# Kernel optimization log

Hardware: AMD Instinct MI355X
Metric: run time of the kernel (lower is better)

The kernel has to match this reference:

```python
import jax, jax.numpy as jnp
import numpy as np

N_NODES = 100000
N_RELS = 237
N_EDGES = 500000
D_IN = 128
D_HID = 128
D_OUT = 128


def setup_inputs() -> dict:
    key = jax.random.key(0)
    ks = jax.random.split(key, 13)
    src = jax.random.randint(ks[0], (N_EDGES,), 0, N_NODES, dtype=jnp.int32)
    dst = jax.random.randint(ks[1], (N_EDGES,), 0, N_NODES, dtype=jnp.int32)
    rel = jax.random.randint(ks[2], (N_EDGES,), 0, N_RELS, dtype=jnp.int32)
    triplets = jnp.stack([src, dst, rel], axis=1)  # [E, 3]
    s = 0.05
    return {
        "triplets": triplets,
        "ent_embed": jax.random.normal(ks[3], (N_NODES, D_IN), jnp.float32) * s,
        "rel_embed": jax.random.normal(ks[4], (N_RELS, D_IN), jnp.float32) * s,
        "W_ent": jax.random.normal(ks[5], (D_IN, D_HID), jnp.float32) * s,
        "b_ent": jnp.zeros((D_HID,), jnp.float32),
        "W_rel": jax.random.normal(ks[6], (D_IN, D_HID), jnp.float32) * s,
        "b_rel": jnp.zeros((D_HID,), jnp.float32),
        "W_ent2": jax.random.normal(ks[7], (3 * D_HID, D_OUT), jnp.float32) * s,
        "b_ent2": jnp.zeros((D_OUT,), jnp.float32),
        "a_w": jax.random.normal(ks[8], (D_OUT, 1), jnp.float32) * s,
        "a_b": jnp.zeros((1,), jnp.float32),
    }


def reference(triplets, ent_embed, rel_embed, W_ent, b_ent, W_rel, b_rel,
              W_ent2, b_ent2, a_w, a_b):
    src_i, dst_i, rel_i = triplets[:, 0], triplets[:, 1], triplets[:, 2]
    # embedding gathers
    src = ent_embed[src_i]          # [E, D_IN]
    dst = ent_embed[dst_i]          # [E, D_IN]
    rel = rel_embed[rel_i]          # [E, D_IN]
    # shared fc_ent projection on src and dst, fc_rel on rel
    src = src @ W_ent + b_ent       # [E, D_HID]
    dst = dst @ W_ent + b_ent
    rel = rel @ W_rel + b_rel
    # per-edge feature c = fc_ent2(cat([src, dst, rel]))
    c = jnp.concatenate([src, dst, rel], axis=1) @ W_ent2 + b_ent2  # [E, D_OUT]
    # unnormalized exp attention score (leaky_relu slope 0.01, torch default)
    b = jnp.exp(jax.nn.leaky_relu((c @ a_w + a_b)[:, 0], negative_slope=0.01))  # [E]
    # segment softmax over edges sharing a source node
    b_sum = jax.ops.segment_sum(b, src_i, num_segments=N_NODES)  # [N]
    alpha = b / b_sum[src_i]                                     # [E]
    # weighted neighbor aggregation per source node
    h = jax.ops.segment_sum(alpha[:, None] * c, src_i, num_segments=N_NODES)  # [N, D_OUT]
    return h
```

## Files before the change

### kernel.cpp

```cpp
#include <hip/hip_runtime.h>
#include <hip/hip_bf16.h>

#define N_NODES_C 100000
#define N_PAD_C   100096
#define N_RELS_C  237
#define N_EDGES_C 500000
#define D 128

typedef __attribute__((ext_vector_type(8))) short short8;
typedef __attribute__((ext_vector_type(4))) float f32x4;

__device__ __forceinline__ ushort f2bf(float x) {
    union { float f; uint u; } v; v.f = x;
    uint r = v.u + 0x7FFFu + ((v.u >> 16) & 1u);
    return (ushort)(r >> 16);
}
__device__ __forceinline__ float bf2f_hi(uint u) {
    union { uint u; float f; } v; v.u = u; return v.f;
}

__global__ void k_fuse_w(const float* __restrict__ W_ent, const float* __restrict__ W_rel,
                         const float* __restrict__ W_ent2,
                         const float* __restrict__ b_ent, const float* __restrict__ b_rel,
                         const float* __restrict__ b_ent2,
                         float* __restrict__ WR, ushort* __restrict__ WfTb,
                         float* __restrict__ biasC) {
    int j = threadIdx.x;
    int k = blockIdx.x;
    int which = blockIdx.y;
    if (which == 0) {
        float acc = 0.f;
        for (int i = 0; i < D; ++i) acc += W_ent[k*D+i] * W_ent2[i*D+j];
        WfTb[j*D + k] = f2bf(acc);
    } else if (which == 1) {
        float acc = 0.f;
        for (int i = 0; i < D; ++i) acc += W_ent[k*D+i] * W_ent2[(D+i)*D+j];
        WfTb[(D+j)*D + k] = f2bf(acc);
    } else if (which == 2) {
        float acc = 0.f;
        for (int i = 0; i < D; ++i) acc += W_rel[k*D+i] * W_ent2[(2*D+i)*D+j];
        WR[k*D + j] = acc;
    } else if (k == 0) {
        float acc = b_ent2[j];
        for (int i = 0; i < D; ++i) {
            acc += b_ent[i] * (W_ent2[i*D+j] + W_ent2[(D+i)*D+j]);
            acc += b_rel[i] * W_ent2[(2*D+i)*D+j];
        }
        biasC[j] = acc;
    }
}

__global__ void k_rel_scalars(const float* __restrict__ rel_embed,
                              const float* __restrict__ a_w, const float* __restrict__ a_b,
                              const float* __restrict__ WR, const float* __restrict__ biasC,
                              float* __restrict__ Rm, float* __restrict__ sR,
                              float* __restrict__ sConst) {
    int j = threadIdx.x;
    int b = blockIdx.x;
    __shared__ float red[128];
    if (b < N_RELS_C) {
        float acc = 0.f;
        for (int k = 0; k < D; ++k) acc += rel_embed[b*D+k] * WR[k*D+j];
        Rm[b*D+j] = acc;
        red[j] = acc * a_w[j];
        __syncthreads();
        for (int s = 64; s > 0; s >>= 1) { if (j < s) red[j] += red[j+s]; __syncthreads(); }
        if (j == 0) sR[b] = red[0];
    } else {
        red[j] = biasC[j] * a_w[j];
        __syncthreads();
        for (int s = 64; s > 0; s >>= 1) { if (j < s) red[j] += red[j+s]; __syncthreads(); }
        if (j == 0) sConst[0] = red[0] + a_b[0];
    }
}

__global__ __launch_bounds__(512, 4) void k1_mfma(const float* __restrict__ ent,
                                                  const ushort* __restrict__ WfTb,
                                                  const float* __restrict__ a_w,
                                                  ushort* __restrict__ AnB,
                                                  ushort* __restrict__ BnB,
                                                  float* __restrict__ sA,
                                                  float* __restrict__ sB,
                                                  int n_nodes) {
    __shared__ __align__(16) ushort wL[256*128];
    int tid = threadIdx.x;
    int m0 = blockIdx.x * 128;

#pragma unroll
    for (int u = 0; u < 8; ++u) {
        int f = u*512 + tid;
        int r = f >> 4, k16 = f & 15;
        *(uint4*)&wL[r*128 + ((k16 ^ (r & 15)) << 3)] =
            *(const uint4*)&WfTb[r*128 + (k16 << 3)];
    }
    __syncthreads();

    int wave = tid >> 6, lane = tid & 63;
    int ny = wave >> 2;
    int q = lane >> 4, c = lane & 15;
    int wm = (wave & 3) * 32;

    f32x4 acc[2][8];
#pragma unroll
    for (int mt = 0; mt < 2; ++mt)
#pragma unroll
        for (int nt = 0; nt < 8; ++nt) { f32x4 z = {0.f,0.f,0.f,0.f}; acc[mt][nt] = z; }

#pragma unroll
    for (int chunk = 0; chunk < 4; ++chunk) {
        int k16 = chunk*4 + q;
        short8 a[2];
#pragma unroll
        for (int mt = 0; mt < 2; ++mt) {
            int row = m0 + wm + mt*16 + c;
            float4 e0 = make_float4(0.f,0.f,0.f,0.f), e1 = e0;
            if (row < n_nodes) {
                const float* ep = &ent[(size_t)row*D + (k16 << 3)];
                e0 = *(const float4*)ep;
                e1 = *(const float4*)(ep + 4);
            }
            short8 pk;
            pk[0]=(short)f2bf(e0.x); pk[1]=(short)f2bf(e0.y); pk[2]=(short)f2bf(e0.z); pk[3]=(short)f2bf(e0.w);
            pk[4]=(short)f2bf(e1.x); pk[5]=(short)f2bf(e1.y); pk[6]=(short)f2bf(e1.z); pk[7]=(short)f2bf(e1.w);
            a[mt] = pk;
        }
#pragma unroll
        for (int nt = 0; nt < 8; ++nt) {
            int wrow = ny*128 + nt*16 + c;
            short8 b = *(const short8*)&wL[wrow*128 + ((k16 ^ c) << 3)];
            acc[0][nt] = __builtin_amdgcn_mfma_f32_16x16x32_bf16(a[0], b, acc[0][nt], 0, 0, 0);
            acc[1][nt] = __builtin_amdgcn_mfma_f32_16x16x32_bf16(a[1], b, acc[1][nt], 0, 0, 0);
        }
    }

    float aw[8];
#pragma unroll
    for (int nt = 0; nt < 8; ++nt) aw[nt] = a_w[nt*16 + c];

    ushort* out  = ny ? BnB : AnB;
    float*  sOut = ny ? sB  : sA;

#pragma unroll
    for (int mt = 0; mt < 2; ++mt) {
#pragma unroll
        for (int reg = 0; reg < 4; ++reg) {
            int m = m0 + wm + mt*16 + q*4 + reg;
            float pa = 0.f;
#pragma unroll
            for (int nt = 0; nt < 8; ++nt) pa += acc[mt][nt][reg] * aw[nt];
#pragma unroll
            for (int msk = 1; msk < 16; msk <<= 1) pa += __shfl_xor(pa, msk);
            if (m < n_nodes) {
                if (c == 0) sOut[m] = pa;
#pragma unroll
                for (int nt = 0; nt < 8; ++nt)
                    out[(size_t)m*D + nt*16 + c] = f2bf(acc[mt][nt][reg]);
            }
        }
    }
}

__global__ void k_hist(const int* __restrict__ trip, int* __restrict__ deg, int n_edges) {
    int e = blockIdx.x*256 + threadIdx.x;
    if (e >= n_edges) return;
    int s = trip[3*e];
    if ((unsigned)s >= (unsigned)N_NODES_C) return;
    atomicAdd(&deg[s], 1);
}

__global__ void k_scan1(const int* __restrict__ deg, int* __restrict__ off,
                        int* __restrict__ bsum, int n) {
    __shared__ int s[1024];
    int i = blockIdx.x*1024 + threadIdx.x;
    int v = (i < n) ? deg[i] : 0;
    s[threadIdx.x] = v; __syncthreads();
    for (int d = 1; d < 1024; d <<= 1) {
        int t = (threadIdx.x >= d) ? s[threadIdx.x - d] : 0;
        __syncthreads();
        s[threadIdx.x] += t;
        __syncthreads();
    }
    if (i < n) off[i] = s[threadIdx.x] - v;
    if (threadIdx.x == 1023) bsum[blockIdx.x] = s[1023];
}

__global__ void k_scan2(int* __restrict__ bsum, int nb) {
    __shared__ int s[128];
    int v = (threadIdx.x < nb) ? bsum[threadIdx.x] : 0;
    s[threadIdx.x] = v; __syncthreads();
    for (int d = 1; d < 128; d <<= 1) {
        int t = (threadIdx.x >= d) ? s[threadIdx.x - d] : 0;
        __syncthreads();
        s[threadIdx.x] += t;
        __syncthreads();
    }
    if (threadIdx.x < nb) bsum[threadIdx.x] = s[threadIdx.x] - v;
}

__global__ void k_scan3(int* __restrict__ off, int* __restrict__ cursor,
                        const int* __restrict__ bsum, int n, int total_edges) {
    int i = blockIdx.x*1024 + threadIdx.x;
    if (i < n) {
        int o = off[i] + bsum[blockIdx.x];
        off[i] = o;
        cursor[i] = o;
    }
    if (i == 0) off[n] = total_edges;
}

__global__ void k_edge_b(const int* __restrict__ trip, const float* __restrict__ sA,
                         const float* __restrict__ sB, const float* __restrict__ sR,
                         const float* __restrict__ sConst, int* __restrict__ cursor,
                         uint2* __restrict__ kb, int n_edges) {
    int e = blockIdx.x*256 + threadIdx.x;
    if (e >= n_edges) return;
    int s = trip[3*e], d = trip[3*e+1], r = trip[3*e+2];
    if ((unsigned)s >= (unsigned)N_NODES_C || (unsigned)d >= (unsigned)N_NODES_C ||
        (unsigned)r >= (unsigned)N_RELS_C) return;
    float logit = sA[s] + sB[d] + sR[r] + sConst[0];
    float l = logit > 0.f ? logit : 0.01f*logit;
    float b = expf(l);
    int p = atomicAdd(&cursor[s], 1);
    kb[p] = make_uint2((uint)(d | (r << 20)), __float_as_uint(b));
}

__global__ void k_aggregate(const int* __restrict__ off, const uint2* __restrict__ kb,
                            const ushort* __restrict__ AnB, const ushort* __restrict__ BnB,
                            const float* __restrict__ Rm, const float* __restrict__ biasC,
                            float* __restrict__ h, int n_nodes) {
    int g = threadIdx.x >> 5, lane = threadIdx.x & 31;
    int n = blockIdx.x*8 + g;
    if (n >= n_nodes) return;
    int o0 = off[n], o1 = off[n+1];
    int c = lane*4;
    if (o0 == o1) {
        *(float4*)&h[(size_t)n*D + c] = make_float4(0.f,0.f,0.f,0.f);
        return;
    }
    float s = 0.f;
    for (int p = o0 + lane; p < o1; p += 32) s += __uint_as_float(kb[p].y);
    for (int m = 16; m > 0; m >>= 1) s += __shfl_xor(s, m, 32);
    float inv = 1.f / s;
    uint2 araw = *(const uint2*)&AnB[(size_t)n*D + c];
    float4 bc  = *(const float4*)&biasC[c];
    float4 acc;
    acc.x = bf2f_hi(araw.x << 16)         + bc.x;
    acc.y = bf2f_hi(araw.x & 0xFFFF0000u) + bc.y;
    acc.z = bf2f_hi(araw.y << 16)         + bc.z;
    acc.w = bf2f_hi(araw.y & 0xFFFF0000u) + bc.w;

    int p = o0;
    for (; p + 4 <= o1; p += 4) {
        uint2 kv0 = kb[p+0], kv1 = kb[p+1], kv2 = kb[p+2], kv3 = kb[p+3];
        uint2 g0 = *(const uint2*)&BnB[(size_t)(kv0.x & 0xFFFFF)*D + c];
        uint2 g1 = *(const uint2*)&BnB[(size_t)(kv1.x & 0xFFFFF)*D + c];
        uint2 g2 = *(const uint2*)&BnB[(size_t)(kv2.x & 0xFFFFF)*D + c];
        uint2 g3 = *(const uint2*)&BnB[(size_t)(kv3.x & 0xFFFFF)*D + c];
        float4 r0 = *(const float4*)&Rm[(kv0.x >> 20)*D + c];
        float4 r1 = *(const float4*)&Rm[(kv1.x >> 20)*D + c];
        float4 r2 = *(const float4*)&Rm[(kv2.x >> 20)*D + c];
        float4 r3 = *(const float4*)&Rm[(kv3.x >> 20)*D + c];
        float a0 = __uint_as_float(kv0.y) * inv;
        float a1 = __uint_as_float(kv1.y) * inv;
        float a2 = __uint_as_float(kv2.y) * inv;
        float a3 = __uint_as_float(kv3.y) * inv;
        acc.x += a0*(bf2f_hi(g0.x << 16)         + r0.x)
               + a1*(bf2f_hi(g1.x << 16)         + r1.x)
               + a2*(bf2f_hi(g2.x << 16)         + r2.x)
               + a3*(bf2f_hi(g3.x << 16)         + r3.x);
        acc.y += a0*(bf2f_hi(g0.x & 0xFFFF0000u) + r0.y)
               + a1*(bf2f_hi(g1.x & 0xFFFF0000u) + r1.y)
               + a2*(bf2f_hi(g2.x & 0xFFFF0000u) + r2.y)
               + a3*(bf2f_hi(g3.x & 0xFFFF0000u) + r3.y);
        acc.z += a0*(bf2f_hi(g0.y << 16)         + r0.z)
               + a1*(bf2f_hi(g1.y << 16)         + r1.z)
               + a2*(bf2f_hi(g2.y << 16)         + r2.z)
               + a3*(bf2f_hi(g3.y << 16)         + r3.z);
        acc.w += a0*(bf2f_hi(g0.y & 0xFFFF0000u) + r0.w)
               + a1*(bf2f_hi(g1.y & 0xFFFF0000u) + r1.w)
               + a2*(bf2f_hi(g2.y & 0xFFFF0000u) + r2.w)
               + a3*(bf2f_hi(g3.y & 0xFFFF0000u) + r3.w);
    }
    for (; p < o1; ++p) {
        uint2 kv = kb[p];
        float al = __uint_as_float(kv.y) * inv;
        uint2 braw = *(const uint2*)&BnB[(size_t)(kv.x & 0xFFFFF)*D + c];
        float4 rv  = *(const float4*)&Rm[(kv.x >> 20)*D + c];
        acc.x += al*(bf2f_hi(braw.x << 16)         + rv.x);
        acc.y += al*(bf2f_hi(braw.x & 0xFFFF0000u) + rv.y);
        acc.z += al*(bf2f_hi(braw.y << 16)         + rv.z);
        acc.w += al*(bf2f_hi(braw.y & 0xFFFF0000u) + rv.w);
    }
    *(float4*)&h[(size_t)n*D + c] = acc;
}

extern "C" void kernel_launch(void* const* d_in, const int* in_sizes, int n_in,
                              void* d_out, int out_size, void* d_ws, size_t ws_size,
                              hipStream_t stream) {
    const int*   trip   = (const int*)  d_in[0];
    const float* ent    = (const float*)d_in[1];
    const float* relE   = (const float*)d_in[2];
    const float* W_ent  = (const float*)d_in[3];
    const float* b_ent  = (const float*)d_in[4];
    const float* W_rel  = (const float*)d_in[5];
    const float* b_rel  = (const float*)d_in[6];
    const float* W_ent2 = (const float*)d_in[7];
    const float* b_ent2 = (const float*)d_in[8];
    const float* a_w    = (const float*)d_in[9];
    const float* a_b    = (const float*)d_in[10];
    float* h = (float*)d_out;

    char* ws = (char*)d_ws;
    size_t o = 0;
    auto alloc = [&](size_t bytes) { size_t p = o; o += (bytes + 255) & ~(size_t)255; return p; };
    float*  WR     = (float*) (ws + alloc(128*128*4));
    ushort* WfTb   = (ushort*)(ws + alloc(256*128*2));
    float*  biasC  = (float*) (ws + alloc(128*4));
    float*  Rm     = (float*) (ws + alloc((size_t)N_RELS_C*128*4));
    float*  sR     = (float*) (ws + alloc(N_RELS_C*4));
    float*  sConst = (float*) (ws + alloc(4));
    float*  sA     = (float*) (ws + alloc((size_t)N_NODES_C*4));
    float*  sB     = (float*) (ws + alloc((size_t)N_NODES_C*4));
    int*    deg    = (int*)   (ws + alloc((size_t)N_NODES_C*4));
    int*    off    = (int*)   (ws + alloc(((size_t)N_NODES_C+1)*4));
    int*    cursor = (int*)   (ws + alloc((size_t)N_NODES_C*4));
    int*    bsum   = (int*)   (ws + alloc(128*4));
    uint2*  kb     = (uint2*) (ws + alloc((size_t)N_EDGES_C*8));
    ushort* BnB    = (ushort*)(ws + alloc((size_t)N_PAD_C*128*2));
    ushort* AnB    = (ushort*)(ws + alloc((size_t)N_PAD_C*128*2));

    hipMemsetAsync(deg, 0, (size_t)N_NODES_C*4, stream);

    k_fuse_w<<<dim3(128,4), 128, 0, stream>>>(W_ent, W_rel, W_ent2, b_ent, b_rel, b_ent2,
                                              WR, WfTb, biasC);
    k_rel_scalars<<<N_RELS_C+1, 128, 0, stream>>>(relE, a_w, a_b, WR, biasC,
                                                  Rm, sR, sConst);
    k1_mfma<<<N_PAD_C/128, 512, 0, stream>>>(ent, WfTb, a_w, AnB, BnB, sA, sB, N_NODES_C);
    k_hist<<<(N_EDGES_C+255)/256, 256, 0, stream>>>(trip, deg, N_EDGES_C);
    int nb = (N_NODES_C + 1023)/1024;
    k_scan1<<<nb, 1024, 0, stream>>>(deg, off, bsum, N_NODES_C);
    k_scan2<<<1, 128, 0, stream>>>(bsum, nb);
    k_scan3<<<nb, 1024, 0, stream>>>(off, cursor, bsum, N_NODES_C, N_EDGES_C);
    k_edge_b<<<(N_EDGES_C+255)/256, 256, 0, stream>>>(trip, sA, sB, sR, sConst,
                                                      cursor, kb, N_EDGES_C);
    k_aggregate<<<(N_NODES_C+7)/8, 256, 0, stream>>>(off, kb, AnB, BnB, Rm, biasC,
                                                     h, N_NODES_C);
}
```

Before: 248.2 us.

## Fuse softmax exp into aggregation, bf16 relation table, 16 lanes per node

The edge kernel now stores only the partial logit sB[d]+sR[r]. The aggregation kernel adds the per-node term, applies leaky-relu and exp, and accumulates numerator and denominator in a single pass, so the separate sum pass over kb is gone. The relation matrix is stored as bf16 to halve gather bytes. Each node now uses 16 lanes with 8 columns apiece and 128-bit loads. The cost is exp computed redundantly by every lane and slightly lower precision in the relation term.

```diff
diff --git a/kernel.cpp b/kernel.cpp
--- a/kernel.cpp
+++ b/kernel.cpp
@@ -53,7 +53,7 @@
 __global__ void k_rel_scalars(const float* __restrict__ rel_embed,
                               const float* __restrict__ a_w, const float* __restrict__ a_b,
                               const float* __restrict__ WR, const float* __restrict__ biasC,
-                              float* __restrict__ Rm, float* __restrict__ sR,
+                              ushort* __restrict__ RmB, float* __restrict__ sR,
                               float* __restrict__ sConst) {
     int j = threadIdx.x;
     int b = blockIdx.x;
@@ -61,7 +61,7 @@
     if (b < N_RELS_C) {
         float acc = 0.f;
         for (int k = 0; k < D; ++k) acc += rel_embed[b*D+k] * WR[k*D+j];
-        Rm[b*D+j] = acc;
+        RmB[b*D+j] = f2bf(acc);
         red[j] = acc * a_w[j];
         __syncthreads();
         for (int s = 64; s > 0; s >>= 1) { if (j < s) red[j] += red[j+s]; __syncthreads(); }
@@ -208,90 +208,99 @@
     if (i == 0) off[n] = total_edges;
 }
 
-__global__ void k_edge_b(const int* __restrict__ trip, const float* __restrict__ sA,
-                         const float* __restrict__ sB, const float* __restrict__ sR,
-                         const float* __restrict__ sConst, int* __restrict__ cursor,
+__global__ void k_edge_b(const int* __restrict__ trip, const float* __restrict__ sB,
+                         const float* __restrict__ sR, int* __restrict__ cursor,
                          uint2* __restrict__ kb, int n_edges) {
     int e = blockIdx.x*256 + threadIdx.x;
     if (e >= n_edges) return;
     int s = trip[3*e], d = trip[3*e+1], r = trip[3*e+2];
     if ((unsigned)s >= (unsigned)N_NODES_C || (unsigned)d >= (unsigned)N_NODES_C ||
         (unsigned)r >= (unsigned)N_RELS_C) return;
-    float logit = sA[s] + sB[d] + sR[r] + sConst[0];
-    float l = logit > 0.f ? logit : 0.01f*logit;
-    float b = expf(l);
+    float v = sB[d] + sR[r];
     int p = atomicAdd(&cursor[s], 1);
-    kb[p] = make_uint2((uint)(d | (r << 20)), __float_as_uint(b));
+    kb[p] = make_uint2((uint)(d | (r << 20)), __float_as_uint(v));
 }
 
 __global__ void k_aggregate(const int* __restrict__ off, const uint2* __restrict__ kb,
                             const ushort* __restrict__ AnB, const ushort* __restrict__ BnB,
-                            const float* __restrict__ Rm, const float* __restrict__ biasC,
+                            const ushort* __restrict__ RmB, const float* __restrict__ biasC,
+                            const float* __restrict__ sA, const float* __restrict__ sConst,
                             float* __restrict__ h, int n_nodes) {
-    int g = threadIdx.x >> 5, lane = threadIdx.x & 31;
-    int n = blockIdx.x*8 + g;
+    int g = threadIdx.x >> 4, lane = threadIdx.x & 15;
+    int n = blockIdx.x*16 + g;
     if (n >= n_nodes) return;
     int o0 = off[n], o1 = off[n+1];
-    int c = lane*4;
+    int c = lane*8;
+    float* hp = &h[(size_t)n*D + c];
     if (o0 == o1) {
-        *(float4*)&h[(size_t)n*D + c] = make_float4(0.f,0.f,0.f,0.f);
+        *(float4*)hp     = make_float4(0.f,0.f,0.f,0.f);
+        *(float4*)(hp+4) = make_float4(0.f,0.f,0.f,0.f);
         return;
     }
-    float s = 0.f;
-    for (int p = o0 + lane; p < o1; p += 32) s += __uint_as_float(kb[p].y);
-    for (int m = 16; m > 0; m >>= 1) s += __shfl_xor(s, m, 32);
-    float inv = 1.f / s;
-    uint2 araw = *(const uint2*)&AnB[(size_t)n*D + c];
-    float4 bc  = *(const float4*)&biasC[c];
-    float4 acc;
-    acc.x = bf2f_hi(araw.x << 16)         + bc.x;
-    acc.y = bf2f_hi(araw.x & 0xFFFF0000u) + bc.y;
-    acc.z = bf2f_hi(araw.y << 16)         + bc.z;
-    acc.w = bf2f_hi(araw.y & 0xFFFF0000u) + bc.w;
+    float t = sA[n] + sConst[0];
+    float num[8];
+#pragma unroll
+    for (int i = 0; i < 8; ++i) num[i] = 0.f;
+    float den = 0.f;
 
     int p = o0;
     for (; p + 4 <= o1; p += 4) {
-        uint2 kv0 = kb[p+0], kv1 = kb[p+1], kv2 = kb[p+2], kv3 = kb[p+3];
-        uint2 g0 = *(const uint2*)&BnB[(size_t)(kv0.x & 0xFFFFF)*D + c];
-        uint2 g1 = *(const uint2*)&BnB[(size_t)(kv1.x & 0xFFFFF)*D + c];
-        uint2 g2 = *(const uint2*)&BnB[(size_t)(kv2.x & 0xFFFFF)*D + c];
-        uint2 g3 = *(const uint2*)&BnB[(size_t)(kv3.x & 0xFFFFF)*D + c];
-        float4 r0 = *(const float4*)&Rm[(kv0.x >> 20)*D + c];
-        float4 r1 = *(const float4*)&Rm[(kv1.x >> 20)*D + c];
-        float4 r2 = *(const float4*)&Rm[(kv2.x >> 20)*D + c];
-        float4 r3 = *(const float4*)&Rm[(kv3.x >> 20)*D + c];
-        float a0 = __uint_as_float(kv0.y) * inv;
-        float a1 = __uint_as_float(kv1.y) * inv;
-        float a2 = __uint_as_float(kv2.y) * inv;
-        float a3 = __uint_as_float(kv3.y) * inv;
-        acc.x += a0*(bf2f_hi(g0.x << 16)         + r0.x)
-               + a1*(bf2f_hi(g1.x << 16)         + r1.x)
-               + a2*(bf2f_hi(g2.x << 16)         + r2.x)
-               + a3*(bf2f_hi(g3.x << 16)         + r3.x);
-        acc.y += a0*(bf2f_hi(g0.x & 0xFFFF0000u) + r0.y)
-               + a1*(bf2f_hi(g1.x & 0xFFFF0000u) + r1.y)
-               + a2*(bf2f_hi(g2.x & 0xFFFF0000u) + r2.y)
-               + a3*(bf2f_hi(g3.x & 0xFFFF0000u) + r3.y);
-        acc.z += a0*(bf2f_hi(g0.y << 16)         + r0.z)
-               + a1*(bf2f_hi(g1.y << 16)         + r1.z)
-               + a2*(bf2f_hi(g2.y << 16)         + r2.z)
-               + a3*(bf2f_hi(g3.y << 16)         + r3.z);
-        acc.w += a0*(bf2f_hi(g0.y & 0xFFFF0000u) + r0.w)
-               + a1*(bf2f_hi(g1.y & 0xFFFF0000u) + r1.w)
-               + a2*(bf2f_hi(g2.y & 0xFFFF0000u) + r2.w)
-               + a3*(bf2f_hi(g3.y & 0xFFFF0000u) + r3.w);
+        uint2 kv[4]; uint4 gB[4], gR[4];
+#pragma unroll
+        for (int u = 0; u < 4; ++u) kv[u] = kb[p+u];
+#pragma unroll
+        for (int u = 0; u < 4; ++u) {
+            gB[u] = *(const uint4*)&BnB[(size_t)(kv[u].x & 0xFFFFF)*D + c];
+            gR[u] = *(const uint4*)&RmB[(size_t)(kv[u].x >> 20)*D + c];
+        }
+#pragma unroll
+        for (int u = 0; u < 4; ++u) {
+            float logit = t + __uint_as_float(kv[u].y);
+            float l = logit > 0.f ? logit : 0.01f*logit;
+            float b = expf(l);
+            den += b;
+            const uint* bu = (const uint*)&gB[u];
+            const uint* ru = (const uint*)&gR[u];
+#pragma unroll
+            for (int i = 0; i < 4; ++i) {
+                num[2*i]   += b * (bf2f_hi(bu[i] << 16)         + bf2f_hi(ru[i] << 16));
+                num[2*i+1] += b * (bf2f_hi(bu[i] & 0xFFFF0000u) + bf2f_hi(ru[i] & 0xFFFF0000u));
+            }
+        }
     }
     for (; p < o1; ++p) {
         uint2 kv = kb[p];
-        float al = __uint_as_float(kv.y) * inv;
-        uint2 braw = *(const uint2*)&BnB[(size_t)(kv.x & 0xFFFFF)*D + c];
-        float4 rv  = *(const float4*)&Rm[(kv.x >> 20)*D + c];
-        acc.x += al*(bf2f_hi(braw.x << 16)         + rv.x);
-        acc.y += al*(bf2f_hi(braw.x & 0xFFFF0000u) + rv.y);
-        acc.z += al*(bf2f_hi(braw.y << 16)         + rv.z);
-        acc.w += al*(bf2f_hi(braw.y & 0xFFFF0000u) + rv.w);
-    }
-    *(float4*)&h[(size_t)n*D + c] = acc;
+        float logit = t + __uint_as_float(kv.y);
+        float l = logit > 0.f ? logit : 0.01f*logit;
+        float b = expf(l);
+        den += b;
+        uint4 gB = *(const uint4*)&BnB[(size_t)(kv.x & 0xFFFFF)*D + c];
+        uint4 gR = *(const uint4*)&RmB[(size_t)(kv.x >> 20)*D + c];
+        const uint* bu = (const uint*)&gB;
+        const uint* ru = (const uint*)&gR;
+#pragma unroll
+        for (int i = 0; i < 4; ++i) {
+            num[2*i]   += b * (bf2f_hi(bu[i] << 16)         + bf2f_hi(ru[i] << 16));
+            num[2*i+1] += b * (bf2f_hi(bu[i] & 0xFFFF0000u) + bf2f_hi(ru[i] & 0xFFFF0000u));
+        }
+    }
+
+    float inv = 1.f / den;
+    uint4 araw = *(const uint4*)&AnB[(size_t)n*D + c];
+    const uint* au = (const uint*)&araw;
+    float4 bc0 = *(const float4*)&biasC[c];
+    float4 bc1 = *(const float4*)&biasC[c+4];
+    float4 o0v, o1v;
+    o0v.x = bf2f_hi(au[0] << 16)         + bc0.x + num[0]*inv;
+    o0v.y = bf2f_hi(au[0] & 0xFFFF0000u) + bc0.y + num[1]*inv;
+    o0v.z = bf2f_hi(au[1] << 16)         + bc0.z + num[2]*inv;
+    o0v.w = bf2f_hi(au[1] & 0xFFFF0000u) + bc0.w + num[3]*inv;
+    o1v.x = bf2f_hi(au[2] << 16)         + bc1.x + num[4]*inv;
+    o1v.y = bf2f_hi(au[2] & 0xFFFF0000u) + bc1.y + num[5]*inv;
+    o1v.z = bf2f_hi(au[3] << 16)         + bc1.z + num[6]*inv;
+    o1v.w = bf2f_hi(au[3] & 0xFFFF0000u) + bc1.w + num[7]*inv;
+    *(float4*)hp     = o0v;
+    *(float4*)(hp+4) = o1v;
 }
 
 extern "C" void kernel_launch(void* const* d_in, const int* in_sizes, int n_in,
@@ -316,7 +325,7 @@
     float*  WR     = (float*) (ws + alloc(128*128*4));
     ushort* WfTb   = (ushort*)(ws + alloc(256*128*2));
     float*  biasC  = (float*) (ws + alloc(128*4));
-    float*  Rm     = (float*) (ws + alloc((size_t)N_RELS_C*128*4));
+    ushort* RmB    = (ushort*)(ws + alloc((size_t)N_RELS_C*128*2));
     float*  sR     = (float*) (ws + alloc(N_RELS_C*4));
     float*  sConst = (float*) (ws + alloc(4));
     float*  sA     = (float*) (ws + alloc((size_t)N_NODES_C*4));
@@ -334,15 +343,14 @@
     k_fuse_w<<<dim3(128,4), 128, 0, stream>>>(W_ent, W_rel, W_ent2, b_ent, b_rel, b_ent2,
                                               WR, WfTb, biasC);
     k_rel_scalars<<<N_RELS_C+1, 128, 0, stream>>>(relE, a_w, a_b, WR, biasC,
-                                                  Rm, sR, sConst);
+                                                  RmB, sR, sConst);
     k1_mfma<<<N_PAD_C/128, 512, 0, stream>>>(ent, WfTb, a_w, AnB, BnB, sA, sB, N_NODES_C);
     k_hist<<<(N_EDGES_C+255)/256, 256, 0, stream>>>(trip, deg, N_EDGES_C);
     int nb = (N_NODES_C + 1023)/1024;
     k_scan1<<<nb, 1024, 0, stream>>>(deg, off, bsum, N_NODES_C);
     k_scan2<<<1, 128, 0, stream>>>(bsum, nb);
     k_scan3<<<nb, 1024, 0, stream>>>(off, cursor, bsum, N_NODES_C, N_EDGES_C);
-    k_edge_b<<<(N_EDGES_C+255)/256, 256, 0, stream>>>(trip, sA, sB, sR, sConst,
-                                                      cursor, kb, N_EDGES_C);
-    k_aggregate<<<(N_NODES_C+7)/8, 256, 0, stream>>>(off, kb, AnB, BnB, Rm, biasC,
-                                                     h, N_NODES_C);
-}
+    k_edge_b<<<(N_EDGES_C+255)/256, 256, 0, stream>>>(trip, sB, sR, cursor, kb, N_EDGES_C);
+    k_aggregate<<<(N_NODES_C+15)/16, 256, 0, stream>>>(off, kb, AnB, BnB, RmB, biasC,
+                                                       sA, sConst, h, N_NODES_C);
+}
```

Result: no change. 244.6 us (-1.5%).
